# Kernel optimization log

Hardware: AMD Instinct MI355X
Metric: run time of the kernel (lower is better)

The kernel has to match this reference:

```python
import jax, jax.numpy as jnp
import numpy as np

N_NODES = 50000
N_EDGES = 800000
N_GRAPHS = 512
NEG_SLOPE = 0.2  # PyG GATv2Conv default negative_slope

# layer dims: (in_feat, out_channels, heads)
LAYER_DIMS = [(11, 64, 3), (192, 64, 3), (192, 64, 3), (192, 20, 1)]


def setup_inputs() -> dict:
    key = jax.random.key(0)
    ks = jax.random.split(key, 4 + 6 * len(LAYER_DIMS))
    inp = {}
    inp["x"] = jax.random.normal(ks[0], (N_NODES, 11), jnp.float32)
    src = jax.random.randint(ks[1], (N_EDGES,), 0, N_NODES, dtype=jnp.int32)
    dst = jax.random.randint(ks[2], (N_EDGES,), 0, N_NODES, dtype=jnp.int32)
    inp["edge_index"] = jnp.stack([src, dst])
    inp["batch"] = jnp.sort(jax.random.randint(ks[3], (N_NODES,), 0, N_GRAPHS, dtype=jnp.int32))
    ki = 4
    for li, (fi, ch, h) in enumerate(LAYER_DIMS):
        fo = h * ch
        s = 1.0 / np.sqrt(fi)
        inp[f"Wl{li}"] = jax.random.normal(ks[ki + 0], (fo, fi), jnp.float32) * s
        inp[f"bl{li}"] = jnp.zeros((fo,), jnp.float32)
        inp[f"Wr{li}"] = jax.random.normal(ks[ki + 1], (fo, fi), jnp.float32) * s
        inp[f"br{li}"] = jnp.zeros((fo,), jnp.float32)
        inp[f"att{li}"] = jax.random.normal(ks[ki + 2], (h, ch), jnp.float32) * (1.0 / np.sqrt(ch))
        inp[f"b{li}"] = jnp.zeros((fo,), jnp.float32)
        ki += 6
    return inp


def gatv2_layer(x, src, dst, Wl, bl, Wr, br, att, bias, heads, ch):
    """PyG GATv2Conv (concat=True): e = att . leaky_relu(lin_l(x_j)+lin_r(x_i)),
    alpha = softmax over incoming edges of each dst node, out = sum alpha * lin_l(x_j)."""
    N = x.shape[0]
    xl = (x @ Wl.T + bl).reshape(N, heads, ch)  # source transform [N,H,C]
    xr = (x @ Wr.T + br).reshape(N, heads, ch)  # target transform [N,H,C]
    m = xl[src] + xr[dst]                        # [E,H,C] edge-wise gather
    e = jnp.einsum("ehc,hc->eh", jax.nn.leaky_relu(m, NEG_SLOPE), att)  # [E,H]
    emax = jax.ops.segment_max(e, dst, num_segments=N)   # per-dst softmax (stable)
    p = jnp.exp(e - emax[dst])
    denom = jax.ops.segment_sum(p, dst, num_segments=N)
    alpha = p / denom[dst]                        # [E,H]
    out = jax.ops.segment_sum(xl[src] * alpha[..., None], dst, num_segments=N)
    return out.reshape(N, heads * ch) + bias


def reference(x, edge_index, batch,
              Wl0, bl0, Wr0, br0, att0, b0,
              Wl1, bl1, Wr1, br1, att1, b1,
              Wl2, bl2, Wr2, br2, att2, b2,
              Wl3, bl3, Wr3, br3, att3, b3):
    N = x.shape[0]
    loop = jnp.arange(N, dtype=edge_index.dtype)  # add_self_loops=True
    src = jnp.concatenate([edge_index[0], loop])
    dst = jnp.concatenate([edge_index[1], loop])
    h = gatv2_layer(x, src, dst, Wl0, bl0, Wr0, br0, att0, b0, 3, 64)
    h = jax.nn.relu(h)
    h = gatv2_layer(h, src, dst, Wl1, bl1, Wr1, br1, att1, b1, 3, 64)
    h = jax.nn.relu(h)
    h = gatv2_layer(h, src, dst, Wl2, bl2, Wr2, br2, att2, b2, 3, 64)
    h = jax.nn.relu(h)
    h = gatv2_layer(h, src, dst, Wl3, bl3, Wr3, br3, att3, b3, 1, 20)
    # global_add_pool
    return jax.ops.segment_sum(h, batch, num_segments=N_GRAPHS)  # [G, 20]
```

## Files before the change

### kernel.cpp

```cpp
#include <hip/hip_runtime.h>

#define NN 50000
#define NE 800000
#define NT 850000
#define NG 512
#define NSB 49

typedef __attribute__((ext_vector_type(8))) short bf16x8;
typedef __attribute__((ext_vector_type(4))) float f32x4;


template <int CTRL>
__device__ __forceinline__ float dpp_add(float x) {
  int y = __builtin_amdgcn_update_dpp(0, __float_as_int(x), CTRL, 0xF, 0xF, true);
  return x + __int_as_float(y);
}
template <int CTRL>
__device__ __forceinline__ float dpp_max(float x) {
  int y = __builtin_amdgcn_update_dpp(0, __float_as_int(x), CTRL, 0xF, 0xF, true);
  return fmaxf(x, __int_as_float(y));
}

__device__ __forceinline__ float swz16(float x) {
  return __int_as_float(__builtin_amdgcn_ds_swizzle(__float_as_int(x), 0x401F));
}

__device__ __forceinline__ float rowsum16(float x) {
  x = dpp_add<0xB1>(x);
  x = dpp_add<0x4E>(x);
  x = dpp_add<0x124>(x);
  x = dpp_add<0x128>(x);
  return x;
}
__device__ __forceinline__ float quadsum4(float x) {
  x = dpp_add<0xB1>(x);
  x = dpp_add<0x4E>(x);
  return x;
}
__device__ __forceinline__ float xg_sum(float x) {
  x += swz16(x);
  auto p = __builtin_amdgcn_permlane32_swap(__float_as_uint(x), __float_as_uint(x), false, false);
  return __uint_as_float(p[0]) + __uint_as_float(p[1]);
}
__device__ __forceinline__ float xg_max(float x) {
  x = fmaxf(x, swz16(x));
  auto p = __builtin_amdgcn_permlane32_swap(__float_as_uint(x), __float_as_uint(x), false, false);
  return fmaxf(__uint_as_float(p[0]), __uint_as_float(p[1]));
}
__device__ __forceinline__ float xq_sum(float x) {
  x = dpp_add<0x124>(x);
  x = dpp_add<0x128>(x);
  return xg_sum(x);
}
__device__ __forceinline__ float xq_max(float x) {
  x = dpp_max<0x124>(x);
  x = dpp_max<0x128>(x);
  return xg_max(x);
}

__device__ __forceinline__ float exp2_fast(float x) {
#if __has_builtin(__builtin_amdgcn_exp2f)
  return __builtin_amdgcn_exp2f(x);
#else
  return exp2f(x);
#endif
}

__device__ __forceinline__ float lrelu(float t) { return fmaxf(t, 0.2f * t); }

__device__ __forceinline__ unsigned int f2bf(float f) {
  unsigned int u = __float_as_uint(f);
  u = (u + 0x7FFFu + ((u >> 16) & 1u)) >> 16;
  return u;
}
__device__ __forceinline__ float bf_lo(unsigned int u) { return __uint_as_float(u << 16); }
__device__ __forceinline__ float bf_hi(unsigned int u) { return __uint_as_float(u & 0xFFFF0000u); }
__device__ __forceinline__ float4 bf2f4(uint2 u) {
  return make_float4(bf_lo(u.x), bf_hi(u.x), bf_lo(u.y), bf_hi(u.y));
}

__device__ __forceinline__ void pk_l(float2& d, float2 a, float2 b) {
  asm("v_pk_fma_f32 %0, %1, %2, %0 op_sel_hi:[0,1,1]" : "+v"(d) : "v"(a), "v"(b));
}
__device__ __forceinline__ void pk_h(float2& d, float2 a, float2 b) {
  asm("v_pk_fma_f32 %0, %1, %2, %0 op_sel:[1,0,0]" : "+v"(d) : "v"(a), "v"(b));
}


__global__ void k_hist(const int* __restrict__ dst, int* __restrict__ cnt) {
  int i = blockIdx.x * blockDim.x + threadIdx.x;
  if (i < NT) {
    int d = (i < NE) ? dst[i] : (i - NE);
    atomicAdd(&cnt[d], 1);
  }
}

__global__ __launch_bounds__(1024)
void k_scanA(const int* __restrict__ cnt, int* __restrict__ offs, int* __restrict__ bsum) {
  __shared__ int sh[1024];
  int tid = threadIdx.x;
  int idx = blockIdx.x * 1024 + tid;
  int v = (idx < NN) ? cnt[idx] : 0;
  sh[tid] = v;
  __syncthreads();
  for (int off = 1; off < 1024; off <<= 1) {
    int t = (tid >= off) ? sh[tid - off] : 0;
    __syncthreads();
    sh[tid] += t;
    __syncthreads();
  }
  if (idx < NN) offs[idx] = sh[tid] - v;
  if (tid == 1023) bsum[blockIdx.x] = sh[1023];
}

__global__ void k_scanB(int* __restrict__ bsum, int* __restrict__ offs) {
  int tot = 0;
#pragma unroll 7
  for (int i = 0; i < NSB; ++i) {
    int v = bsum[i];
    bsum[i] = tot;
    tot += v;
  }
  offs[NN] = tot;
}

__global__ __launch_bounds__(1024)
void k_scanC(int* __restrict__ offs, const int* __restrict__ bsum) {
  int idx = blockIdx.x * 1024 + threadIdx.x;
  if (idx < NN) offs[idx] += bsum[blockIdx.x];
}

__global__ void k_scatter(const int* __restrict__ src, const int* __restrict__ dst,
                          const int* __restrict__ offs, int* __restrict__ cur,
                          int* __restrict__ srt) {
  int i = blockIdx.x * blockDim.x + threadIdx.x;
  if (i < NT) {
    int s, d;
    if (i < NE) { s = src[i]; d = dst[i]; }
    else        { s = d = i - NE; }
    int pos = offs[d] + atomicAdd(&cur[d], 1);
    srt[pos] = s;
  }
}

__global__ void k_goffs(const int* __restrict__ batch, int* __restrict__ goffs) {
  int i = blockIdx.x * 256 + threadIdx.x;
  if (i >= NN) return;
  int b = batch[i];
  if (i == 0) {
    for (int g = 0; g <= b; ++g) goffs[g] = 0;
  } else {
    int pb = batch[i - 1];
    for (int g = pb + 1; g <= b; ++g) goffs[g] = i;
  }
  if (i == NN - 1) {
    for (int g = b + 1; g <= NG; ++g) goffs[g] = NN;
  }
}


__global__ void k_cvtW(const float* __restrict__ a, const float* __restrict__ b,
                       const float* __restrict__ c, const float* __restrict__ d,
                       const float* __restrict__ e, const float* __restrict__ f,
                       unsigned short* __restrict__ out) {
  int i = blockIdx.x * 256 + threadIdx.x;
  if (i >= 155136) return;
  float v;
  if      (i < 36864)  v = a[i];
  else if (i < 73728)  v = b[i - 36864];
  else if (i < 110592) v = c[i - 73728];
  else if (i < 147456) v = d[i - 110592];
  else if (i < 151296) v = e[i - 147456];
  else                 v = f[i - 151296];
  out[i] = (unsigned short)f2bf(v);
}


__global__ __launch_bounds__(256)
void k_gemm_mfma2(const unsigned short* __restrict__ Abf,
                  const unsigned short* __restrict__ W1bf,
                  const unsigned short* __restrict__ W2bf,
                  const float* __restrict__ bias1, const float* __restrict__ bias2,
                  unsigned short* __restrict__ C1, unsigned short* __restrict__ C2,
                  int M, int FO) {
  int tid = threadIdx.x;
  int l = tid & 63, wid = tid >> 6;
  int mb = blockIdx.x * 64, nb = blockIdx.y * 64;
  int wr = (wid >> 1) * 32, wc = (wid & 1) * 32;
  int lr = l & 15, lk = (l >> 4) * 8;

  int ar0 = min(mb + wr +  0 + lr, M - 1);
  int ar1 = min(mb + wr + 16 + lr, M - 1);
  int bc0 = min(nb + wc +  0 + lr, FO - 1);
  int bc1 = min(nb + wc + 16 + lr, FO - 1);
  const unsigned short* pa0 = Abf  + (size_t)ar0 * 192 + lk;
  const unsigned short* pa1 = Abf  + (size_t)ar1 * 192 + lk;
  const unsigned short* q10 = W1bf + (size_t)bc0 * 192 + lk;
  const unsigned short* q11 = W1bf + (size_t)bc1 * 192 + lk;
  const unsigned short* q20 = W2bf + (size_t)bc0 * 192 + lk;
  const unsigned short* q21 = W2bf + (size_t)bc1 * 192 + lk;

  f32x4 acc[2][2][2];
#pragma unroll
  for (int a = 0; a < 2; ++a)
#pragma unroll
    for (int b = 0; b < 2; ++b)
#pragma unroll
      for (int c = 0; c < 2; ++c) acc[a][b][c] = (f32x4){0.f, 0.f, 0.f, 0.f};

#pragma unroll
  for (int kt = 0; kt < 6; ++kt) {
    bf16x8 a0  = *(const bf16x8*)(pa0 + kt * 32);
    bf16x8 a1  = *(const bf16x8*)(pa1 + kt * 32);
    bf16x8 b10 = *(const bf16x8*)(q10 + kt * 32);
    bf16x8 b11 = *(const bf16x8*)(q11 + kt * 32);
    bf16x8 b20 = *(const bf16x8*)(q20 + kt * 32);
    bf16x8 b21 = *(const bf16x8*)(q21 + kt * 32);
    acc[0][0][0] = __builtin_amdgcn_mfma_f32_16x16x32_bf16(a0, b10, acc[0][0][0], 0, 0, 0);
    acc[0][0][1] = __builtin_amdgcn_mfma_f32_16x16x32_bf16(a0, b11, acc[0][0][1], 0, 0, 0);
    acc[0][1][0] = __builtin_amdgcn_mfma_f32_16x16x32_bf16(a1, b10, acc[0][1][0], 0, 0, 0);
    acc[0][1][1] = __builtin_amdgcn_mfma_f32_16x16x32_bf16(a1, b11, acc[0][1][1], 0, 0, 0);
    acc[1][0][0] = __builtin_amdgcn_mfma_f32_16x16x32_bf16(a0, b20, acc[1][0][0], 0, 0, 0);
    acc[1][0][1] = __builtin_amdgcn_mfma_f32_16x16x32_bf16(a0, b21, acc[1][0][1], 0, 0, 0);
    acc[1][1][0] = __builtin_amdgcn_mfma_f32_16x16x32_bf16(a1, b20, acc[1][1][0], 0, 0, 0);
    acc[1][1][1] = __builtin_amdgcn_mfma_f32_16x16x32_bf16(a1, b21, acc[1][1][1], 0, 0, 0);
  }

  int rb = (l >> 4) * 4;
#pragma unroll
  for (int mt = 0; mt < 2; ++mt) {
    unsigned short* C = mt == 0 ? C1 : C2;
    const float* bias = mt == 0 ? bias1 : bias2;
#pragma unroll
    for (int fn = 0; fn < 2; ++fn) {
      int col = nb + wc + fn * 16 + lr;
      if (col >= FO) continue;
      float bv = bias[col];
#pragma unroll
      for (int fm = 0; fm < 2; ++fm) {
        const f32x4& av = acc[mt][fm][fn];
#pragma unroll
        for (int i = 0; i < 4; ++i) {
          int row = mb + wr + fm * 16 + rb + i;
          if (row < M) C[(size_t)row * FO + col] = (unsigned short)f2bf(av[i] + bv);
        }
      }
    }
  }
}


__global__ __launch_bounds__(256)
void k_gemm_dual(const float* __restrict__ A, int M, int K, int FO,
                 const float* __restrict__ W1, const float* __restrict__ bias1,
                 const float* __restrict__ W2, const float* __restrict__ bias2,
                 unsigned short* __restrict__ C1, unsigned short* __restrict__ C2) {
  constexpr int CT = 16;
  constexpr int BN = CT * 4;
  constexpr int BR = (256 / CT) * 8;
  constexpr int AF4 = BR / 64;
  __shared__ float As[16][BR + 4];
  __shared__ float Bs[2][16][BN + 4];

  int tid = threadIdx.x;
  int tx = tid % CT, ty = tid / CT;
  int mb = blockIdx.x * BR, nb = blockIdx.y * BN;
  int nkt = (K + 15) >> 4;

  float4 sa[AF4], sb1, sb2;

  auto ldrow = [&](const float* P, int row, int lim, int k0, int kq) -> float4 {
    float4 v = make_float4(0.f, 0.f, 0.f, 0.f);
    if (row < lim) {
      float t[4];
#pragma unroll
      for (int i = 0; i < 4; ++i)
        t[i] = (k0 + kq + i < K) ? P[(size_t)row * K + k0 + kq + i] : 0.f;
      v = make_float4(t[0], t[1], t[2], t[3]);
    }
    return v;
  };

  auto loadg = [&](int kt) {
    int k0 = kt * 16;
#pragma unroll
    for (int q = 0; q < AF4; ++q) {
      int f4 = q * 256 + tid;
      sa[q] = ldrow(A, mb + (f4 >> 2), M, k0, (f4 & 3) * 4);
    }
    int row = tid >> 2, kq = (tid & 3) * 4;
    sb1 = ldrow(W1, nb + row, FO, k0, kq);
    sb2 = ldrow(W2, nb + row, FO, k0, kq);
  };

  auto stlds = [&]() {
#pragma unroll
    for (int q = 0; q < AF4; ++q) {
      int f4 = q * 256 + tid;
      int row = f4 >> 2, kq = (f4 & 3) * 4;
      As[kq + 0][row] = sa[q].x; As[kq + 1][row] = sa[q].y;
      As[kq + 2][row] = sa[q].z; As[kq + 3][row] = sa[q].w;
    }
    int row = tid >> 2, kq = (tid & 3) * 4;
    Bs[0][kq + 0][row] = sb1.x; Bs[0][kq + 1][row] = sb1.y;
    Bs[0][kq + 2][row] = sb1.z; Bs[0][kq + 3][row] = sb1.w;
    Bs[1][kq + 0][row] = sb2.x; Bs[1][kq + 1][row] = sb2.y;
    Bs[1][kq + 2][row] = sb2.z; Bs[1][kq + 3][row] = sb2.w;
  };

  float2 c1[8][2], c2[8][2];
#pragma unroll
  for (int r = 0; r < 8; ++r)
#pragma unroll
    for (int j = 0; j < 2; ++j) {
      c1[r][j] = make_float2(0.f, 0.f);
      c2[r][j] = make_float2(0.f, 0.f);
    }

  loadg(0);
  stlds();
  __syncthreads();

  for (int t = 0;;) {
#pragma unroll
    for (int k = 0; k < 16; ++k) {
      float4 av0 = *(const float4*)&As[k][ty * 8 + 0];
      float4 av1 = *(const float4*)&As[k][ty * 8 + 4];
      float4 bv1 = *(const float4*)&Bs[0][k][tx * 4];
      float4 bv2 = *(const float4*)&Bs[1][k][tx * 4];
      float2 f1a = make_float2(bv1.x, bv1.y), f1b = make_float2(bv1.z, bv1.w);
      float2 f2a = make_float2(bv2.x, bv2.y), f2b = make_float2(bv2.z, bv2.w);
      float2 a01 = make_float2(av0.x, av0.y), a23 = make_float2(av0.z, av0.w);
      float2 a45 = make_float2(av1.x, av1.y), a67 = make_float2(av1.z, av1.w);
#define PKROW(rp, a)                                                       \
      pk_l(c1[2 * rp + 0][0], a, f1a); pk_l(c1[2 * rp + 0][1], a, f1b);    \
      pk_h(c1[2 * rp + 1][0], a, f1a); pk_h(c1[2 * rp + 1][1], a, f1b);    \
      pk_l(c2[2 * rp + 0][0], a, f2a); pk_l(c2[2 * rp + 0][1], a, f2b);    \
      pk_h(c2[2 * rp + 1][0], a, f2a); pk_h(c2[2 * rp + 1][1], a, f2b);
      PKROW(0, a01) PKROW(1, a23) PKROW(2, a45) PKROW(3, a67)
#undef PKROW
    }
    if (++t == nkt) break;
    loadg(t);
    __syncthreads();
    stlds();
    __syncthreads();
  }

  int col = nb + tx * 4;
  if (col < FO) {
    float4 bb1 = *(const float4*)&bias1[col];
    float4 bb2 = *(const float4*)&bias2[col];
#pragma unroll
    for (int r = 0; r < 8; ++r) {
      int m = mb + ty * 8 + r;
      if (m >= M) continue;
      uint2 o1, o2;
      o1.x = f2bf(c1[r][0].x + bb1.x) | (f2bf(c1[r][0].y + bb1.y) << 16);
      o1.y = f2bf(c1[r][1].x + bb1.z) | (f2bf(c1[r][1].y + bb1.w) << 16);
      o2.x = f2bf(c2[r][0].x + bb2.x) | (f2bf(c2[r][0].y + bb2.y) << 16);
      o2.y = f2bf(c2[r][1].x + bb2.z) | (f2bf(c2[r][1].y + bb2.w) << 16);
      *(uint2*)&C1[(size_t)m * FO + col] = o1;
      *(uint2*)&C2[(size_t)m * FO + col] = o2;
    }
  }
}


__global__ __launch_bounds__(256)
void k_gat3(const unsigned short* __restrict__ xl, const unsigned short* __restrict__ xr,
            const float* __restrict__ att, const float* __restrict__ bias,
            const int* __restrict__ offs, const int* __restrict__ srt,
            unsigned short* __restrict__ obf, int relu) {
  const float L2E = 1.4426950408889634f;
  int lane = threadIdx.x & 63;
  int grp = lane >> 4, lg = lane & 15;
  int n = blockIdx.x * 4 + (threadIdx.x >> 6);
  if (n >= NN) return;

  float4 xrv[3], atv[3];
#pragma unroll
  for (int h = 0; h < 3; ++h) {
    xrv[h] = bf2f4(*(const uint2*)(xr + (size_t)n * 192 + h * 64 + lg * 4));
    float4 a = *(const float4*)&att[h * 64 + lg * 4];
    atv[h] = make_float4(a.x * L2E, a.y * L2E, a.z * L2E, a.w * L2E);
  }
  float m[3] = {-1e30f, -1e30f, -1e30f}, d[3] = {0.f, 0.f, 0.f};
  float4 acc[3];
#pragma unroll
  for (int h = 0; h < 3; ++h) acc[h] = make_float4(0.f, 0.f, 0.f, 0.f);

  int e0 = offs[n], e1 = offs[n + 1];
  int nch = (e1 - e0 + 3) >> 2;

  uint2 Rc[3];
  bool vc;
  int j = e0 + grp;
  {
    int jj = min(j, e1 - 1);
    int s = srt[jj];
    const unsigned short* b = xl + (size_t)s * 192 + lg * 4;
    Rc[0] = *(const uint2*)(b);
    Rc[1] = *(const uint2*)(b + 64);
    Rc[2] = *(const uint2*)(b + 128);
    vc = j < e1;
  }
  for (int it = 0; it < nch; ++it) {
    uint2 Rn[3];
    bool vn = false;
    int jn = j + 4;
    if (it + 1 < nch) {
      int jj = min(jn, e1 - 1);
      int s = srt[jj];
      const unsigned short* b = xl + (size_t)s * 192 + lg * 4;
      Rn[0] = *(const uint2*)(b);
      Rn[1] = *(const uint2*)(b + 64);
      Rn[2] = *(const uint2*)(b + 128);
      vn = jn < e1;
    }
    float4 Xc[3];
    Xc[0] = bf2f4(Rc[0]); Xc[1] = bf2f4(Rc[1]); Xc[2] = bf2f4(Rc[2]);
    float part[3];
#pragma unroll
    for (int h = 0; h < 3; ++h) {
      float t = lrelu(Xc[h].x + xrv[h].x);
      float pa = t * atv[h].x;
      t = lrelu(Xc[h].y + xrv[h].y); pa = fmaf(t, atv[h].y, pa);
      t = lrelu(Xc[h].z + xrv[h].z); pa = fmaf(t, atv[h].z, pa);
      t = lrelu(Xc[h].w + xrv[h].w); pa = fmaf(t, atv[h].w, pa);
      part[h] = pa;
    }
#pragma unroll
    for (int h = 0; h < 3; ++h) {
      part[h] = rowsum16(part[h]);
      part[h] = vc ? part[h] : -1e30f;
    }
    float g = fmaxf(fmaxf(part[0] - m[0], part[1] - m[1]), part[2] - m[2]);
    if (__any(g > 11.0f)) {
#pragma unroll
      for (int h = 0; h < 3; ++h) {
        float nm = fmaxf(m[h], part[h]);
        float sc = exp2_fast(m[h] - nm);
        d[h] *= sc;
        acc[h].x *= sc; acc[h].y *= sc; acc[h].z *= sc; acc[h].w *= sc;
        m[h] = nm;
      }
    }
#pragma unroll
    for (int h = 0; h < 3; ++h) {
      float p = vc ? exp2_fast(part[h] - m[h]) : 0.f;
      d[h] += p;
      acc[h].x = fmaf(p, Xc[h].x, acc[h].x);
      acc[h].y = fmaf(p, Xc[h].y, acc[h].y);
      acc[h].z = fmaf(p, Xc[h].z, acc[h].z);
      acc[h].w = fmaf(p, Xc[h].w, acc[h].w);
    }
    Rc[0] = Rn[0]; Rc[1] = Rn[1]; Rc[2] = Rn[2];
    vc = vn; j = jn;
  }

#pragma unroll
  for (int h = 0; h < 3; ++h) {
    float nm = xg_max(m[h]);
    float sc = exp2_fast(m[h] - nm);
    float D = xg_sum(d[h] * sc);
    float A0 = xg_sum(acc[h].x * sc);
    float A1 = xg_sum(acc[h].y * sc);
    float A2 = xg_sum(acc[h].z * sc);
    float A3 = xg_sum(acc[h].w * sc);
    if (grp == 0) {
      float4 bb = *(const float4*)&bias[h * 64 + lg * 4];
      float inv = 1.0f / D;
      float v0 = fmaf(A0, inv, bb.x);
      float v1 = fmaf(A1, inv, bb.y);
      float v2 = fmaf(A2, inv, bb.z);
      float v3 = fmaf(A3, inv, bb.w);
      if (relu) {
        v0 = fmaxf(v0, 0.f); v1 = fmaxf(v1, 0.f);
        v2 = fmaxf(v2, 0.f); v3 = fmaxf(v3, 0.f);
      }
      unsigned int lo = f2bf(v0) | (f2bf(v1) << 16);
      unsigned int hi = f2bf(v2) | (f2bf(v3) << 16);
      *(uint2*)(obf + (size_t)n * 192 + h * 64 + lg * 4) = make_uint2(lo, hi);
    }
  }
}


__global__ __launch_bounds__(256)
void k_gat1(const unsigned short* __restrict__ xl, const unsigned short* __restrict__ xr,
            const float* __restrict__ att, const float* __restrict__ bias,
            const int* __restrict__ offs, const int* __restrict__ srt,
            float* __restrict__ hout) {
  const float L2E = 1.4426950408889634f;
  int lane = threadIdx.x & 63;
  int grp = lane >> 2, lg = lane & 3;
  int n = blockIdx.x * 4 + (threadIdx.x >> 6);
  if (n >= NN) return;

  float xrv[5], atv[5];
#pragma unroll
  for (int i = 0; i < 5; ++i) {
    xrv[i] = bf_lo(xr[(size_t)n * 20 + lg * 5 + i]);
    atv[i] = att[lg * 5 + i] * L2E;
  }
  float m = -1e30f, d = 0.f, a[5] = {0.f, 0.f, 0.f, 0.f, 0.f};

  int e0 = offs[n], e1 = offs[n + 1];
  int nch = (e1 - e0 + 15) >> 4;

  float Xc[5];
  bool vc;
  int j = e0 + grp;
  {
    int jj = min(j, e1 - 1);
    int s = srt[jj];
    const unsigned short* b = xl + (size_t)s * 20 + lg * 5;
#pragma unroll
    for (int i = 0; i < 5; ++i) Xc[i] = bf_lo(b[i]);
    vc = j < e1;
  }
  for (int it = 0; it < nch; ++it) {
    float Xn[5] = {0.f, 0.f, 0.f, 0.f, 0.f};
    bool vn = false;
    int jn = j + 16;
    if (it + 1 < nch) {
      int jj = min(jn, e1 - 1);
      int s = srt[jj];
      const unsigned short* b = xl + (size_t)s * 20 + lg * 5;
#pragma unroll
      for (int i = 0; i < 5; ++i) Xn[i] = bf_lo(b[i]);
      vn = jn < e1;
    }
    float pa = lrelu(Xc[0] + xrv[0]) * atv[0];
#pragma unroll
    for (int i = 1; i < 5; ++i) pa = fmaf(lrelu(Xc[i] + xrv[i]), atv[i], pa);
    pa = quadsum4(pa);
    pa = vc ? pa : -1e30f;
    if (__any(pa - m > 11.0f)) {
      float nm = fmaxf(m, pa);
      float sc = exp2_fast(m - nm);
      d *= sc;
#pragma unroll
      for (int i = 0; i < 5; ++i) a[i] *= sc;
      m = nm;
    }
    float p = vc ? exp2_fast(pa - m) : 0.f;
    d += p;
#pragma unroll
    for (int i = 0; i < 5; ++i) a[i] = fmaf(p, Xc[i], a[i]);
#pragma unroll
    for (int i = 0; i < 5; ++i) Xc[i] = Xn[i];
    vc = vn; j = jn;
  }

  float nm = xq_max(m);
  float sc = exp2_fast(m - nm);
  float D = xq_sum(d * sc);
  float A[5];
#pragma unroll
  for (int i = 0; i < 5; ++i) A[i] = xq_sum(a[i] * sc);
  if (grp == 0) {
    float inv = 1.0f / D;
    float* o = hout + (size_t)n * 20 + lg * 5;
#pragma unroll
    for (int i = 0; i < 5; ++i)
      o[i] = fmaf(A[i], inv, bias[lg * 5 + i]);
  }
}


__global__ __launch_bounds__(64)
void k_pool(const float* __restrict__ h, const int* __restrict__ goffs,
            float* __restrict__ out) {
  int g = blockIdx.x;
  int lane = threadIdx.x;
  if (lane >= 20) return;
  int s = goffs[g], e = goffs[g + 1];
  float sum = 0.f;
  for (int r = s; r < e; ++r) sum += h[(size_t)r * 20 + lane];
  out[g * 20 + lane] = sum;
}


extern "C" void kernel_launch(void* const* d_in, const int* in_sizes, int n_in,
                              void* d_out, int out_size, void* d_ws, size_t ws_size,
                              hipStream_t stream) {
  const float* x = (const float*)d_in[0];
  const int* src = (const int*)d_in[1];
  const int* dst = src + NE;
  const int* batch = (const int*)d_in[2];
  const float *Wl[4], *bl[4], *Wr[4], *br[4], *att[4], *bb[4];
  for (int li = 0; li < 4; ++li) {
    Wl[li]  = (const float*)d_in[3 + li * 6 + 0];
    bl[li]  = (const float*)d_in[3 + li * 6 + 1];
    Wr[li]  = (const float*)d_in[3 + li * 6 + 2];
    br[li]  = (const float*)d_in[3 + li * 6 + 3];
    att[li] = (const float*)d_in[3 + li * 6 + 4];
    bb[li]  = (const float*)d_in[3 + li * 6 + 5];
  }

  char* p = (char*)d_ws;
  auto alloc = [&](size_t bytes) {
    char* r = p;
    p += (bytes + 255) & ~(size_t)255;
    return r;
  };
  unsigned short* xlbf = (unsigned short*)alloc((size_t)NN * 192 * 2);
  unsigned short* xrbf = (unsigned short*)alloc((size_t)NN * 192 * 2);
  unsigned short* hbf  = (unsigned short*)alloc((size_t)NN * 192 * 2);
  unsigned short* wb   = (unsigned short*)alloc((size_t)155136 * 2);
  int* srt   = (int*)alloc((size_t)NT * 4);
  int* offs  = (int*)alloc((size_t)(NN + 1) * 4);
  int* cnt   = (int*)alloc((size_t)NN * 4);
  int* cur   = (int*)alloc((size_t)NN * 4);
  int* bsum  = (int*)alloc((size_t)NSB * 4);
  int* goffs = (int*)alloc((size_t)(NG + 1) * 4);
  float* hpool = (float*)alloc((size_t)NN * 20 * 4);

  hipMemsetAsync(cnt, 0, (size_t)NN * 4, stream);
  hipMemsetAsync(cur, 0, (size_t)NN * 4, stream);

  k_hist<<<(NT + 255) / 256, 256, 0, stream>>>(dst, cnt);
  k_scanA<<<NSB, 1024, 0, stream>>>(cnt, offs, bsum);
  k_scanB<<<1, 1, 0, stream>>>(bsum, offs);
  k_scanC<<<NSB, 1024, 0, stream>>>(offs, bsum);
  k_scatter<<<(NT + 255) / 256, 256, 0, stream>>>(src, dst, offs, cur, srt);
  k_goffs<<<(NN + 255) / 256, 256, 0, stream>>>(batch, goffs);
  k_cvtW<<<(155136 + 255) / 256, 256, 0, stream>>>(Wl[1], Wr[1], Wl[2], Wr[2], Wl[3], Wr[3], wb);

  {
    dim3 g((NN + 127) / 128, 3);
    k_gemm_dual<<<g, 256, 0, stream>>>(x, NN, 11, 192, Wl[0], bl[0], Wr[0], br[0], xlbf, xrbf);
    k_gat3<<<(NN + 3) / 4, 256, 0, stream>>>(xlbf, xrbf, att[0], bb[0], offs, srt, hbf, 1);
  }
  {
    dim3 gm((NN + 63) / 64, 3);
    k_gemm_mfma2<<<gm, 256, 0, stream>>>(hbf, wb + 0, wb + 36864, bl[1], br[1], xlbf, xrbf, NN, 192);
    k_gat3<<<(NN + 3) / 4, 256, 0, stream>>>(xlbf, xrbf, att[1], bb[1], offs, srt, hbf, 1);
    k_gemm_mfma2<<<gm, 256, 0, stream>>>(hbf, wb + 73728, wb + 110592, bl[2], br[2], xlbf, xrbf, NN, 192);
    k_gat3<<<(NN + 3) / 4, 256, 0, stream>>>(xlbf, xrbf, att[2], bb[2], offs, srt, hbf, 1);
  }
  {
    dim3 gm((NN + 63) / 64, 1);
    k_gemm_mfma2<<<gm, 256, 0, stream>>>(hbf, wb + 147456, wb + 151296, bl[3], br[3], xlbf, xrbf, NN, 20);
    k_gat1<<<(NN + 3) / 4, 256, 0, stream>>>(xlbf, xrbf, att[3], bb[3], offs, srt, hpool);
    k_pool<<<NG, 64, 0, stream>>>(hpool, goffs, (float*)d_out);
  }
}
```

Before: 534.9 us.

## Merge preprocessing kernels, swap GEMM grid order, pack GAT math into v_pk ops

Three preprocessing kernels (histogram, weight bf16 conversion, graph offsets) are merged into one launch split by block ranges, which removes two launch overheads. The MFMA GEMM grid is transposed so the column-tile index varies fastest, letting the blocks that share an A row tile run close together and reuse it in cache. The GAT inner loop now uses packed f32 add/mul/fma instructions, with leaky-relu rewritten as 0.6*t + 0.4*|t|, to cut VALU instruction count. The rewritten leaky-relu can differ slightly in rounding, and the inline asm may limit compiler scheduling.

Result: slower. 557.3 us (+4.2%).

```diff
diff --git a/kernel.cpp b/kernel.cpp
--- a/kernel.cpp
+++ b/kernel.cpp
@@ -5,6 +5,9 @@
 #define NT 850000
 #define NG 512
 #define NSB 49
+#define HB 3321
+#define CB 606
+#define GB 196
 
 typedef __attribute__((ext_vector_type(8))) short bf16x8;
 typedef __attribute__((ext_vector_type(4))) float f32x4;
@@ -79,6 +82,21 @@
   return make_float4(bf_lo(u.x), bf_hi(u.x), bf_lo(u.y), bf_hi(u.y));
 }
 
+__device__ __forceinline__ float2 pk_add2(float2 a, float2 b) {
+  float2 d;
+  asm("v_pk_add_f32 %0, %1, %2" : "=v"(d) : "v"(a), "v"(b));
+  return d;
+}
+__device__ __forceinline__ float2 pk_mul2(float2 a, float2 b) {
+  float2 d;
+  asm("v_pk_mul_f32 %0, %1, %2" : "=v"(d) : "v"(a), "v"(b));
+  return d;
+}
+__device__ __forceinline__ float2 pk_fma2(float2 a, float2 b, float2 c) {
+  float2 d = c;
+  asm("v_pk_fma_f32 %0, %1, %2, %0" : "+v"(d) : "v"(a), "v"(b));
+  return d;
+}
 __device__ __forceinline__ void pk_l(float2& d, float2 a, float2 b) {
   asm("v_pk_fma_f32 %0, %1, %2, %0 op_sel_hi:[0,1,1]" : "+v"(d) : "v"(a), "v"(b));
 }
@@ -87,13 +105,49 @@
 }
 
 
-__global__ void k_hist(const int* __restrict__ dst, int* __restrict__ cnt) {
-  int i = blockIdx.x * blockDim.x + threadIdx.x;
-  if (i < NT) {
-    int d = (i < NE) ? dst[i] : (i - NE);
-    atomicAdd(&cnt[d], 1);
-  }
-}
+__global__ void k_pre(const int* __restrict__ dst, int* __restrict__ cnt,
+                      const float* __restrict__ wa, const float* __restrict__ wbp,
+                      const float* __restrict__ wc, const float* __restrict__ wd,
+                      const float* __restrict__ we, const float* __restrict__ wf,
+                      unsigned short* __restrict__ wout,
+                      const int* __restrict__ batch, int* __restrict__ goffs) {
+  int b = blockIdx.x;
+  int tid = threadIdx.x;
+  if (b < HB) {
+    int i = b * 256 + tid;
+    if (i < NT) {
+      int d = (i < NE) ? dst[i] : (i - NE);
+      atomicAdd(&cnt[d], 1);
+    }
+  } else if (b < HB + CB) {
+    int i = (b - HB) * 256 + tid;
+    if (i < 155136) {
+      float v;
+      if      (i < 36864)  v = wa[i];
+      else if (i < 73728)  v = wbp[i - 36864];
+      else if (i < 110592) v = wc[i - 73728];
+      else if (i < 147456) v = wd[i - 110592];
+      else if (i < 151296) v = we[i - 147456];
+      else                 v = wf[i - 151296];
+      wout[i] = (unsigned short)f2bf(v);
+    }
+  } else {
+    int i = (b - HB - CB) * 256 + tid;
+    if (i < NN) {
+      int bb = batch[i];
+      if (i == 0) {
+        for (int g = 0; g <= bb; ++g) goffs[g] = 0;
+      } else {
+        int pb = batch[i - 1];
+        for (int g = pb + 1; g <= bb; ++g) goffs[g] = i;
+      }
+      if (i == NN - 1) {
+        for (int g = bb + 1; g <= NG; ++g) goffs[g] = NN;
+      }
+    }
+  }
+}
+
 
 __global__ __launch_bounds__(1024)
 void k_scanA(const int* __restrict__ cnt, int* __restrict__ offs, int* __restrict__ bsum) {
@@ -143,38 +197,6 @@
   }
 }
 
-__global__ void k_goffs(const int* __restrict__ batch, int* __restrict__ goffs) {
-  int i = blockIdx.x * 256 + threadIdx.x;
-  if (i >= NN) return;
-  int b = batch[i];
-  if (i == 0) {
-    for (int g = 0; g <= b; ++g) goffs[g] = 0;
-  } else {
-    int pb = batch[i - 1];
-    for (int g = pb + 1; g <= b; ++g) goffs[g] = i;
-  }
-  if (i == NN - 1) {
-    for (int g = b + 1; g <= NG; ++g) goffs[g] = NN;
-  }
-}
-
-
-__global__ void k_cvtW(const float* __restrict__ a, const float* __restrict__ b,
-                       const float* __restrict__ c, const float* __restrict__ d,
-                       const float* __restrict__ e, const float* __restrict__ f,
-                       unsigned short* __restrict__ out) {
-  int i = blockIdx.x * 256 + threadIdx.x;
-  if (i >= 155136) return;
-  float v;
-  if      (i < 36864)  v = a[i];
-  else if (i < 73728)  v = b[i - 36864];
-  else if (i < 110592) v = c[i - 73728];
-  else if (i < 147456) v = d[i - 110592];
-  else if (i < 151296) v = e[i - 147456];
-  else                 v = f[i - 151296];
-  out[i] = (unsigned short)f2bf(v);
-}
-
 
 __global__ __launch_bounds__(256)
 void k_gemm_mfma2(const unsigned short* __restrict__ Abf,
@@ -185,7 +207,7 @@
                   int M, int FO) {
   int tid = threadIdx.x;
   int l = tid & 63, wid = tid >> 6;
-  int mb = blockIdx.x * 64, nb = blockIdx.y * 64;
+  int mb = blockIdx.y * 64, nb = blockIdx.x * 64;
   int wr = (wid >> 1) * 32, wc = (wid & 1) * 32;
   int lr = l & 15, lk = (l >> 4) * 8;
 
@@ -377,18 +399,23 @@
   int grp = lane >> 4, lg = lane & 15;
   int n = blockIdx.x * 4 + (threadIdx.x >> 6);
   if (n >= NN) return;
-
-  float4 xrv[3], atv[3];
+  const float2 C06 = make_float2(0.6f, 0.6f);
+  const float2 C04 = make_float2(0.4f, 0.4f);
+
+  float2 xrp[6], atp[6];
 #pragma unroll
   for (int h = 0; h < 3; ++h) {
-    xrv[h] = bf2f4(*(const uint2*)(xr + (size_t)n * 192 + h * 64 + lg * 4));
+    uint2 u = *(const uint2*)(xr + (size_t)n * 192 + h * 64 + lg * 4);
+    xrp[h * 2 + 0] = make_float2(bf_lo(u.x), bf_hi(u.x));
+    xrp[h * 2 + 1] = make_float2(bf_lo(u.y), bf_hi(u.y));
     float4 a = *(const float4*)&att[h * 64 + lg * 4];
-    atv[h] = make_float4(a.x * L2E, a.y * L2E, a.z * L2E, a.w * L2E);
-  }
-  float m[3] = {-1e30f, -1e30f, -1e30f}, d[3] = {0.f, 0.f, 0.f};
-  float4 acc[3];
-#pragma unroll
-  for (int h = 0; h < 3; ++h) acc[h] = make_float4(0.f, 0.f, 0.f, 0.f);
+    atp[h * 2 + 0] = make_float2(a.x * L2E, a.y * L2E);
+    atp[h * 2 + 1] = make_float2(a.z * L2E, a.w * L2E);
+  }
+  float m[3] = {-1e30f, -1e30f, -1e30f}, dd[3] = {0.f, 0.f, 0.f};
+  float2 ac[6];
+#pragma unroll
+  for (int i = 0; i < 6; ++i) ac[i] = make_float2(0.f, 0.f);
 
   int e0 = offs[n], e1 = offs[n + 1];
   int nch = (e1 - e0 + 3) >> 2;
@@ -418,17 +445,21 @@
       Rn[2] = *(const uint2*)(b + 128);
       vn = jn < e1;
     }
-    float4 Xc[3];
-    Xc[0] = bf2f4(Rc[0]); Xc[1] = bf2f4(Rc[1]); Xc[2] = bf2f4(Rc[2]);
+    float2 X[6];
     float part[3];
 #pragma unroll
     for (int h = 0; h < 3; ++h) {
-      float t = lrelu(Xc[h].x + xrv[h].x);
-      float pa = t * atv[h].x;
-      t = lrelu(Xc[h].y + xrv[h].y); pa = fmaf(t, atv[h].y, pa);
-      t = lrelu(Xc[h].z + xrv[h].z); pa = fmaf(t, atv[h].z, pa);
-      t = lrelu(Xc[h].w + xrv[h].w); pa = fmaf(t, atv[h].w, pa);
-      part[h] = pa;
+      X[h * 2 + 0] = make_float2(bf_lo(Rc[h].x), bf_hi(Rc[h].x));
+      X[h * 2 + 1] = make_float2(bf_lo(Rc[h].y), bf_hi(Rc[h].y));
+      float2 t0 = pk_add2(X[h * 2 + 0], xrp[h * 2 + 0]);
+      float2 t1 = pk_add2(X[h * 2 + 1], xrp[h * 2 + 1]);
+      float2 b0 = make_float2(fabsf(t0.x), fabsf(t0.y));
+      float2 b1 = make_float2(fabsf(t1.x), fabsf(t1.y));
+      float2 l0 = pk_fma2(t0, C06, pk_mul2(b0, C04));
+      float2 l1 = pk_fma2(t1, C06, pk_mul2(b1, C04));
+      float2 ps = pk_mul2(l0, atp[h * 2 + 0]);
+      ps = pk_fma2(l1, atp[h * 2 + 1], ps);
+      part[h] = ps.x + ps.y;
     }
 #pragma unroll
     for (int h = 0; h < 3; ++h) {
@@ -441,19 +472,19 @@
       for (int h = 0; h < 3; ++h) {
         float nm = fmaxf(m[h], part[h]);
         float sc = exp2_fast(m[h] - nm);
-        d[h] *= sc;
-        acc[h].x *= sc; acc[h].y *= sc; acc[h].z *= sc; acc[h].w *= sc;
+        dd[h] *= sc;
+        ac[h * 2 + 0].x *= sc; ac[h * 2 + 0].y *= sc;
+        ac[h * 2 + 1].x *= sc; ac[h * 2 + 1].y *= sc;
         m[h] = nm;
       }
     }
 #pragma unroll
     for (int h = 0; h < 3; ++h) {
       float p = vc ? exp2_fast(part[h] - m[h]) : 0.f;
-      d[h] += p;
-      acc[h].x = fmaf(p, Xc[h].x, acc[h].x);
-      acc[h].y = fmaf(p, Xc[h].y, acc[h].y);
-      acc[h].z = fmaf(p, Xc[h].z, acc[h].z);
-      acc[h].w = fmaf(p, Xc[h].w, acc[h].w);
+      dd[h] += p;
+      float2 P = make_float2(p, p);
+      pk_l(ac[h * 2 + 0], P, X[h * 2 + 0]);
+      pk_l(ac[h * 2 + 1], P, X[h * 2 + 1]);
     }
     Rc[0] = Rn[0]; Rc[1] = Rn[1]; Rc[2] = Rn[2];
     vc = vn; j = jn;
@@ -463,11 +494,11 @@
   for (int h = 0; h < 3; ++h) {
     float nm = xg_max(m[h]);
     float sc = exp2_fast(m[h] - nm);
-    float D = xg_sum(d[h] * sc);
-    float A0 = xg_sum(acc[h].x * sc);
-    float A1 = xg_sum(acc[h].y * sc);
-    float A2 = xg_sum(acc[h].z * sc);
-    float A3 = xg_sum(acc[h].w * sc);
+    float D  = xg_sum(dd[h] * sc);
+    float A0 = xg_sum(ac[h * 2 + 0].x * sc);
+    float A1 = xg_sum(ac[h * 2 + 0].y * sc);
+    float A2 = xg_sum(ac[h * 2 + 1].x * sc);
+    float A3 = xg_sum(ac[h * 2 + 1].y * sc);
     if (grp == 0) {
       float4 bb = *(const float4*)&bias[h * 64 + lg * 4];
       float inv = 1.0f / D;
@@ -621,13 +652,13 @@
   hipMemsetAsync(cnt, 0, (size_t)NN * 4, stream);
   hipMemsetAsync(cur, 0, (size_t)NN * 4, stream);
 
-  k_hist<<<(NT + 255) / 256, 256, 0, stream>>>(dst, cnt);
+  k_pre<<<HB + CB + GB, 256, 0, stream>>>(dst, cnt,
+                                          Wl[1], Wr[1], Wl[2], Wr[2], Wl[3], Wr[3], wb,
+                                          batch, goffs);
   k_scanA<<<NSB, 1024, 0, stream>>>(cnt, offs, bsum);
   k_scanB<<<1, 1, 0, stream>>>(bsum, offs);
   k_scanC<<<NSB, 1024, 0, stream>>>(offs, bsum);
   k_scatter<<<(NT + 255) / 256, 256, 0, stream>>>(src, dst, offs, cur, srt);
-  k_goffs<<<(NN + 255) / 256, 256, 0, stream>>>(batch, goffs);
-  k_cvtW<<<(155136 + 255) / 256, 256, 0, stream>>>(Wl[1], Wr[1], Wl[2], Wr[2], Wl[3], Wr[3], wb);
 
   {
     dim3 g((NN + 127) / 128, 3);
@@ -635,14 +666,14 @@
     k_gat3<<<(NN + 3) / 4, 256, 0, stream>>>(xlbf, xrbf, att[0], bb[0], offs, srt, hbf, 1);
   }
   {
-    dim3 gm((NN + 63) / 64, 3);
+    dim3 gm(3, (NN + 63) / 64);
     k_gemm_mfma2<<<gm, 256, 0, stream>>>(hbf, wb + 0, wb + 36864, bl[1], br[1], xlbf, xrbf, NN, 192);
     k_gat3<<<(NN + 3) / 4, 256, 0, stream>>>(xlbf, xrbf, att[1], bb[1], offs, srt, hbf, 1);
     k_gemm_mfma2<<<gm, 256, 0, stream>>>(hbf, wb + 73728, wb + 110592, bl[2], br[2], xlbf, xrbf, NN, 192);
     k_gat3<<<(NN + 3) / 4, 256, 0, stream>>>(xlbf, xrbf, att[2], bb[2], offs, srt, hbf, 1);
   }
   {
-    dim3 gm((NN + 63) / 64, 1);
+    dim3 gm(1, (NN + 63) / 64);
     k_gemm_mfma2<<<gm, 256, 0, stream>>>(hbf, wb + 147456, wb + 151296, bl[3], br[3], xlbf, xrbf, NN, 20);
     k_gat1<<<(NN + 3) / 4, 256, 0, stream>>>(xlbf, xrbf, att[3], bb[3], offs, srt, hpool);
     k_pool<<<NG, 64, 0, stream>>>(hpool, goffs, (float*)d_out);
```
